# Performance work log

Hardware: AMD Instinct MI355X
Metric: run time of the kernel (lower is better)

## Reference

```python
import jax, jax.numpy as jnp
import numpy as np


def setup_inputs() -> dict:
    key = jax.random.key(0)
    k1, k2 = jax.random.split(key)
    batch, d_model, L = 4096, 1024, 2048
    # binary inputs in {0,1} as in torch.randint(0, 2, ...)
    x = jax.random.randint(k1, (batch, L), 0, 2, dtype=jnp.int32)
    references = jax.random.randint(k2, (d_model, L), 0, 2).astype(jnp.float32)
    return {"x": x, "references": references}


def reference(x, references):
    # Hamming distance between binary vectors a,b in {0,1}:
    #   sum(a != b) = sum(a) + sum(b) - 2 * a.b
    # This avoids materializing the (batch, d_model, L) broadcast tensor
    # while computing exactly the same values as the original module.
    L = x.shape[-1]
    xf = x.astype(jnp.float32)                     # (B, L)
    dot = jnp.einsum('bl,dl->bd', xf, references)  # (B, D)
    sum_x = jnp.sum(xf, axis=-1, keepdims=True)    # (B, 1)
    sum_r = jnp.sum(references, axis=-1)           # (D,)
    hamming = sum_x + sum_r[None, :] - 2.0 * dot   # (B, D)
    mean = L / 2
    std = 0.5 * (L ** 0.5)
    return (hamming - mean) / std
```

## Files before the change

### kernel.cpp

```cpp
#include <hip/hip_runtime.h>
#include <stdint.h>

constexpr int B_ROWS = 4096;
constexpr int D_ROWS = 1024;
constexpr int L_LEN  = 2048;

using int32x4 = __attribute__((ext_vector_type(4))) int;

__global__ __launch_bounds__(256) void convert_kernel(
    const int* __restrict__ x, const float* __restrict__ r,
    uint32_t* __restrict__ xq, uint32_t* __restrict__ rq,
    int groups_x, int groups_total)
{
  const int tid = blockIdx.x * blockDim.x + threadIdx.x;
  const int nth = gridDim.x * blockDim.x;
  for (int g = tid; g < groups_total; g += nth) {
    if (g < groups_x) {
      const int4 v = *reinterpret_cast<const int4*>(x + (size_t)g * 4);
      const uint32_t b0 = v.x ? 0xFFu : 0x01u;
      const uint32_t b1 = v.y ? 0xFFu : 0x01u;
      const uint32_t b2 = v.z ? 0xFFu : 0x01u;
      const uint32_t b3 = v.w ? 0xFFu : 0x01u;
      xq[g] = b0 | (b1 << 8) | (b2 << 16) | (b3 << 24);
    } else {
      const int gr = g - groups_x;
      const float4 v = *reinterpret_cast<const float4*>(r + (size_t)gr * 4);
      const uint32_t b0 = (v.x != 0.0f) ? 0xFFu : 0x01u;
      const uint32_t b1 = (v.y != 0.0f) ? 0xFFu : 0x01u;
      const uint32_t b2 = (v.z != 0.0f) ? 0xFFu : 0x01u;
      const uint32_t b3 = (v.w != 0.0f) ? 0xFFu : 0x01u;
      rq[gr] = b0 | (b1 << 8) | (b2 << 16) | (b3 << 24);
    }
  }
}

constexpr int BM = 64;
constexpr int BN = 64;
constexpr int BK = 128;
constexpr int KSTEPS = L_LEN / BK;
constexpr int GRID_D = D_ROWS / BN;
constexpr int NWG    = (B_ROWS / BM) * GRID_D;

typedef __attribute__((address_space(3))) void       as3_void;
typedef const __attribute__((address_space(1))) void as1_cvoid;

__device__ __forceinline__ void gload_lds16(const void* g, void* l) {
  __builtin_amdgcn_global_load_lds((as1_cvoid*)g, (as3_void*)l, 16, 0, 0);
}

__global__ __launch_bounds__(256, 4) void gemm_i8_kernel(
    const char* __restrict__ Aq, const char* __restrict__ Bq,
    float* __restrict__ out)
{
  __shared__ __align__(16) char A_lds[2][BM * BK];
  __shared__ __align__(16) char B_lds[2][BN * BK];

  const int lin = blockIdx.x;
  const int swz = (lin & 7) * (NWG / 8) + (lin >> 3);
  const int bm  = (swz / GRID_D) * BM;
  const int bn  = (swz % GRID_D) * BN;

  const int t    = threadIdx.x;
  const int lane = t & 63;
  const int w    = t >> 6;
  const int wr   = w >> 1;
  const int wc   = w & 1;

  const int l8  = lane >> 3;
  const int c16 = lane & 7;

  const char* gA[2];
  const char* gB[2];
#pragma unroll
  for (int c = 0; c < 2; ++c) {
    const int r = w * 16 + c * 8 + l8;
    gA[c] = Aq + (size_t)(bm + r) * L_LEN + ((c16 ^ (r & 7)) * 16);
    gB[c] = Bq + (size_t)(bn + r) * L_LEN + ((c16 ^ (r & 7)) * 16);
  }

#define STAGE(buf, k0) do {                                                   \
    _Pragma("unroll") for (int _c = 0; _c < 2; ++_c)                          \
      gload_lds16(gA[_c] + (k0), A_lds[buf] + (w * 16 + _c * 8) * BK);        \
    _Pragma("unroll") for (int _c = 0; _c < 2; ++_c)                          \
      gload_lds16(gB[_c] + (k0), B_lds[buf] + (w * 16 + _c * 8) * BK);        \
  } while (0)

  int32x4 acc[2][2] = {};

  STAGE(0, 0);
  __syncthreads();

  for (int ks = 0; ks < KSTEPS; ++ks) {
    const int cur = ks & 1;
    if (ks + 1 < KSTEPS) STAGE(cur ^ 1, (ks + 1) * BK);

    int32x4 a[2][2], b[2][2];
#pragma unroll
    for (int kk = 0; kk < 2; ++kk) {
      const int kcol = kk * 64 + (lane >> 4) * 16;
#pragma unroll
      for (int f = 0; f < 2; ++f) {
        const int row = wr * 32 + f * 16 + (lane & 15);
        a[f][kk] = *reinterpret_cast<const int32x4*>(
            A_lds[cur] + row * BK + (kcol ^ ((row & 7) << 4)));
      }
#pragma unroll
      for (int gg = 0; gg < 2; ++gg) {
        const int row = wc * 32 + gg * 16 + (lane & 15);
        b[gg][kk] = *reinterpret_cast<const int32x4*>(
            B_lds[cur] + row * BK + (kcol ^ ((row & 7) << 4)));
      }
    }
#pragma unroll
    for (int kk = 0; kk < 2; ++kk)
#pragma unroll
      for (int f = 0; f < 2; ++f)
#pragma unroll
        for (int gg = 0; gg < 2; ++gg)
          acc[f][gg] = __builtin_amdgcn_mfma_i32_16x16x64_i8(
              a[f][kk], b[gg][kk], acc[f][gg], 0, 0, 0);

    __syncthreads();
  }
#undef STAGE

  const float scale = -0.5f * 0.04419417382415922f;
#pragma unroll
  for (int f = 0; f < 2; ++f) {
    const int brow = bm + wr * 32 + f * 16 + (lane >> 4) * 4;
#pragma unroll
    for (int gg = 0; gg < 2; ++gg) {
      const int d = bn + wc * 32 + gg * 16 + (lane & 15);
#pragma unroll
      for (int reg = 0; reg < 4; ++reg)
        out[(size_t)(brow + reg) * D_ROWS + d] = (float)acc[f][gg][reg] * scale;
    }
  }
}

extern "C" void kernel_launch(void* const* d_in, const int* in_sizes, int n_in,
                              void* d_out, int out_size, void* d_ws, size_t ws_size,
                              hipStream_t stream) {
  const int*   x = (const int*)d_in[0];
  const float* r = (const float*)d_in[1];
  float*     out = (float*)d_out;

  char* Aq = (char*)d_ws;
  char* Bq = Aq + (size_t)B_ROWS * L_LEN;

  const int groups_x = B_ROWS * L_LEN / 4;
  const int groups_r = D_ROWS * L_LEN / 4;
  const int groups_total = groups_x + groups_r;

  convert_kernel<<<2048, 256, 0, stream>>>(
      x, r, (uint32_t*)Aq, (uint32_t*)Bq, groups_x, groups_total);

  gemm_i8_kernel<<<NWG, 256, 0, stream>>>(Aq, Bq, out);
}
```

Baseline: 31.00 us.

## Switch binary GEMM from int8 to FP4 scaled MFMA with larger tiles

Encodes the ±1 binary inputs as FP4 e2m1 nibbles (+1/-1) instead of int8 bytes, which halves the workspace and global-to-LDS traffic. The GEMM now uses the 32x32x64 f8f6f4 scaled MFMA in FP4 mode with unit scales. The M tile grows to 128 with a reworked LDS swizzle and load mapping. The FP32 accumulation stays exact for these small integer sums. The catch is a new register layout and epilogue mapping, plus the launch bound no longer asking for 4 blocks per CU.

```diff
diff --git a/kernel.cpp b/kernel.cpp
--- a/kernel.cpp
+++ b/kernel.cpp
@@ -4,10 +4,13 @@
 constexpr int B_ROWS = 4096;
 constexpr int D_ROWS = 1024;
 constexpr int L_LEN  = 2048;
+constexpr int LB     = L_LEN / 2;
 
 using int32x4 = __attribute__((ext_vector_type(4))) int;
+using int32x8 = __attribute__((ext_vector_type(8))) int;
+using f32x16  = __attribute__((ext_vector_type(16))) float;
 
-__global__ __launch_bounds__(256) void convert_kernel(
+__global__ __launch_bounds__(256) void convert_fp4_kernel(
     const int* __restrict__ x, const float* __restrict__ r,
     uint32_t* __restrict__ xq, uint32_t* __restrict__ rq,
     int groups_x, int groups_total)
@@ -15,31 +18,42 @@
   const int tid = blockIdx.x * blockDim.x + threadIdx.x;
   const int nth = gridDim.x * blockDim.x;
   for (int g = tid; g < groups_total; g += nth) {
+    uint32_t wo;
     if (g < groups_x) {
-      const int4 v = *reinterpret_cast<const int4*>(x + (size_t)g * 4);
-      const uint32_t b0 = v.x ? 0xFFu : 0x01u;
-      const uint32_t b1 = v.y ? 0xFFu : 0x01u;
-      const uint32_t b2 = v.z ? 0xFFu : 0x01u;
-      const uint32_t b3 = v.w ? 0xFFu : 0x01u;
-      xq[g] = b0 | (b1 << 8) | (b2 << 16) | (b3 << 24);
+      const int4 v0 = *reinterpret_cast<const int4*>(x + (size_t)g * 8);
+      const int4 v1 = *reinterpret_cast<const int4*>(x + (size_t)g * 8 + 4);
+      wo  = (v0.x ? 0xAu : 0x2u);
+      wo |= (v0.y ? 0xAu : 0x2u) << 4;
+      wo |= (v0.z ? 0xAu : 0x2u) << 8;
+      wo |= (v0.w ? 0xAu : 0x2u) << 12;
+      wo |= (v1.x ? 0xAu : 0x2u) << 16;
+      wo |= (v1.y ? 0xAu : 0x2u) << 20;
+      wo |= (v1.z ? 0xAu : 0x2u) << 24;
+      wo |= (v1.w ? 0xAu : 0x2u) << 28;
+      xq[g] = wo;
     } else {
       const int gr = g - groups_x;
-      const float4 v = *reinterpret_cast<const float4*>(r + (size_t)gr * 4);
-      const uint32_t b0 = (v.x != 0.0f) ? 0xFFu : 0x01u;
-      const uint32_t b1 = (v.y != 0.0f) ? 0xFFu : 0x01u;
-      const uint32_t b2 = (v.z != 0.0f) ? 0xFFu : 0x01u;
-      const uint32_t b3 = (v.w != 0.0f) ? 0xFFu : 0x01u;
-      rq[gr] = b0 | (b1 << 8) | (b2 << 16) | (b3 << 24);
+      const float4 v0 = *reinterpret_cast<const float4*>(r + (size_t)gr * 8);
+      const float4 v1 = *reinterpret_cast<const float4*>(r + (size_t)gr * 8 + 4);
+      wo  = (v0.x != 0.0f ? 0xAu : 0x2u);
+      wo |= (v0.y != 0.0f ? 0xAu : 0x2u) << 4;
+      wo |= (v0.z != 0.0f ? 0xAu : 0x2u) << 8;
+      wo |= (v0.w != 0.0f ? 0xAu : 0x2u) << 12;
+      wo |= (v1.x != 0.0f ? 0xAu : 0x2u) << 16;
+      wo |= (v1.y != 0.0f ? 0xAu : 0x2u) << 20;
+      wo |= (v1.z != 0.0f ? 0xAu : 0x2u) << 24;
+      wo |= (v1.w != 0.0f ? 0xAu : 0x2u) << 28;
+      rq[gr] = wo;
     }
   }
 }
 
-constexpr int BM = 64;
+constexpr int BM = 128;
 constexpr int BN = 64;
-constexpr int BK = 128;
-constexpr int KSTEPS = L_LEN / BK;
+constexpr int BKB = 64;
+constexpr int KSTEPS = LB / BKB;
 constexpr int GRID_D = D_ROWS / BN;
-constexpr int NWG    = (B_ROWS / BM) * GRID_D;
+constexpr int NWG = (B_ROWS / BM) * GRID_D;
 
 typedef __attribute__((address_space(3))) void       as3_void;
 typedef const __attribute__((address_space(1))) void as1_cvoid;
@@ -48,12 +62,12 @@
   __builtin_amdgcn_global_load_lds((as1_cvoid*)g, (as3_void*)l, 16, 0, 0);
 }
 
-__global__ __launch_bounds__(256, 4) void gemm_i8_kernel(
-    const char* __restrict__ Aq, const char* __restrict__ Bq,
+__global__ __launch_bounds__(256) void gemm_fp4_kernel(
+    const uint8_t* __restrict__ Aq, const uint8_t* __restrict__ Bq,
     float* __restrict__ out)
 {
-  __shared__ __align__(16) char A_lds[2][BM * BK];
-  __shared__ __align__(16) char B_lds[2][BN * BK];
+  __shared__ __align__(16) uint8_t A_lds[2][BM * BKB];
+  __shared__ __align__(16) uint8_t B_lds[2][BN * BKB];
 
   const int lin = blockIdx.x;
   const int swz = (lin & 7) * (NWG / 8) + (lin >> 3);
@@ -66,74 +80,62 @@
   const int wr   = w >> 1;
   const int wc   = w & 1;
 
-  const int l8  = lane >> 3;
-  const int c16 = lane & 7;
-
-  const char* gA[2];
-  const char* gB[2];
+  const uint8_t* gA[2];
 #pragma unroll
   for (int c = 0; c < 2; ++c) {
-    const int r = w * 16 + c * 8 + l8;
-    gA[c] = Aq + (size_t)(bm + r) * L_LEN + ((c16 ^ (r & 7)) * 16);
-    gB[c] = Bq + (size_t)(bn + r) * L_LEN + ((c16 ^ (r & 7)) * 16);
+    const int r = w * 32 + c * 16 + (lane >> 2);
+    gA[c] = Aq + (size_t)(bm + r) * LB + (((lane & 3) ^ ((r >> 1) & 3)) * 16);
   }
+  const int rB = w * 16 + (lane >> 2);
+  const uint8_t* gB0 =
+      Bq + (size_t)(bn + rB) * LB + (((lane & 3) ^ ((rB >> 1) & 3)) * 16);
 
-#define STAGE(buf, k0) do {                                                   \
+#define STAGE(buf, k0b) do {                                                  \
     _Pragma("unroll") for (int _c = 0; _c < 2; ++_c)                          \
-      gload_lds16(gA[_c] + (k0), A_lds[buf] + (w * 16 + _c * 8) * BK);        \
-    _Pragma("unroll") for (int _c = 0; _c < 2; ++_c)                          \
-      gload_lds16(gB[_c] + (k0), B_lds[buf] + (w * 16 + _c * 8) * BK);        \
+      gload_lds16(gA[_c] + (k0b), A_lds[buf] + (w * 32 + _c * 16) * BKB);     \
+    gload_lds16(gB0 + (k0b), B_lds[buf] + (w * 16) * BKB);                    \
   } while (0)
 
-  int32x4 acc[2][2] = {};
+  f32x16 acc[2] = {};
 
   STAGE(0, 0);
   __syncthreads();
 
   for (int ks = 0; ks < KSTEPS; ++ks) {
     const int cur = ks & 1;
-    if (ks + 1 < KSTEPS) STAGE(cur ^ 1, (ks + 1) * BK);
+    if (ks + 1 < KSTEPS) STAGE(cur ^ 1, (ks + 1) * BKB);
 
-    int32x4 a[2][2], b[2][2];
 #pragma unroll
-    for (int kk = 0; kk < 2; ++kk) {
-      const int kcol = kk * 64 + (lane >> 4) * 16;
+    for (int kc = 0; kc < 2; ++kc) {
+      const int rowB  = wc * 32 + (lane & 31);
+      const int qB    = 2 * kc + (lane >> 5);
+      const int32x4 b4 = *reinterpret_cast<const int32x4*>(
+          B_lds[cur] + rowB * BKB + ((qB ^ ((rowB >> 1) & 3)) * 16));
+      const int32x8 b8 = {b4[0], b4[1], b4[2], b4[3], 0, 0, 0, 0};
 #pragma unroll
       for (int f = 0; f < 2; ++f) {
-        const int row = wr * 32 + f * 16 + (lane & 15);
-        a[f][kk] = *reinterpret_cast<const int32x4*>(
-            A_lds[cur] + row * BK + (kcol ^ ((row & 7) << 4)));
-      }
-#pragma unroll
-      for (int gg = 0; gg < 2; ++gg) {
-        const int row = wc * 32 + gg * 16 + (lane & 15);
-        b[gg][kk] = *reinterpret_cast<const int32x4*>(
-            B_lds[cur] + row * BK + (kcol ^ ((row & 7) << 4)));
+        const int rowA  = wr * 64 + f * 32 + (lane & 31);
+        const int qA    = 2 * kc + (lane >> 5);
+        const int32x4 a4 = *reinterpret_cast<const int32x4*>(
+            A_lds[cur] + rowA * BKB + ((qA ^ ((rowA >> 1) & 3)) * 16));
+        const int32x8 a8 = {a4[0], a4[1], a4[2], a4[3], 0, 0, 0, 0};
+        acc[f] = __builtin_amdgcn_mfma_scale_f32_32x32x64_f8f6f4(
+            a8, b8, acc[f], 4, 4, 0, 0x7F7F7F7F, 0, 0x7F7F7F7F);
       }
     }
-#pragma unroll
-    for (int kk = 0; kk < 2; ++kk)
-#pragma unroll
-      for (int f = 0; f < 2; ++f)
-#pragma unroll
-        for (int gg = 0; gg < 2; ++gg)
-          acc[f][gg] = __builtin_amdgcn_mfma_i32_16x16x64_i8(
-              a[f][kk], b[gg][kk], acc[f][gg], 0, 0, 0);
-
     __syncthreads();
   }
 #undef STAGE
 
   const float scale = -0.5f * 0.04419417382415922f;
+  const int col = bn + wc * 32 + (lane & 31);
 #pragma unroll
   for (int f = 0; f < 2; ++f) {
-    const int brow = bm + wr * 32 + f * 16 + (lane >> 4) * 4;
 #pragma unroll
-    for (int gg = 0; gg < 2; ++gg) {
-      const int d = bn + wc * 32 + gg * 16 + (lane & 15);
-#pragma unroll
-      for (int reg = 0; reg < 4; ++reg)
-        out[(size_t)(brow + reg) * D_ROWS + d] = (float)acc[f][gg][reg] * scale;
+    for (int reg = 0; reg < 16; ++reg) {
+      const int row = bm + wr * 64 + f * 32 + (reg & 3) + 8 * (reg >> 2)
+                    + 4 * (lane >> 5);
+      out[(size_t)row * D_ROWS + col] = acc[f][reg] * scale;
     }
   }
 }
@@ -145,15 +147,15 @@
   const float* r = (const float*)d_in[1];
   float*     out = (float*)d_out;
 
-  char* Aq = (char*)d_ws;
-  char* Bq = Aq + (size_t)B_ROWS * L_LEN;
+  uint8_t* Aq = (uint8_t*)d_ws;
+  uint8_t* Bq = Aq + (size_t)B_ROWS * LB;
 
-  const int groups_x = B_ROWS * L_LEN / 4;
-  const int groups_r = D_ROWS * L_LEN / 4;
+  const int groups_x = B_ROWS * L_LEN / 8;
+  const int groups_r = D_ROWS * L_LEN / 8;
   const int groups_total = groups_x + groups_r;
 
-  convert_kernel<<<2048, 256, 0, stream>>>(
+  convert_fp4_kernel<<<2048, 256, 0, stream>>>(
       x, r, (uint32_t*)Aq, (uint32_t*)Bq, groups_x, groups_total);
 
-  gemm_i8_kernel<<<NWG, 256, 0, stream>>>(Aq, Bq, out);
+  gemm_fp4_kernel<<<NWG, 256, 0, stream>>>(Aq, Bq, out);
 }
```

Result: faster. 27.38 us (-11.7%).
